# Performance work log

Hardware: AMD Instinct MI355X
Metric: run time of the kernel (lower is better)

The kernel has to match this reference:

```python
import jax, jax.numpy as jnp
import numpy as np

PRUNE_N, PRUNE_M = 2, 4
RIA_A = 1.0
NUM_HEADS = 16
HEAD_DIM = 128
ROPE_THETA = 10000.0


def sparse_mask(W, scaler_row, perm):
    # RIA metric: |W|/colsum + |W|/rowsum, scaled by sqrt(scaler_row)**a
    absW = jnp.abs(W)
    metric = (absW / absW.sum(axis=0, keepdims=True)
              + absW / absW.sum(axis=1, keepdims=True))
    metric = metric * (jnp.sqrt(scaler_row)[None, :] ** RIA_A)
    Wm = metric @ perm                      # permute columns: [R, C]
    R, C = Wm.shape
    nb = C // PRUNE_M
    blocks = Wm.reshape(R, nb, PRUNE_M)
    # hard N:M mask: top-n per block of m
    _, idx = jax.lax.top_k(blocks, PRUNE_N)           # [R, nb, n]
    hard = jax.nn.one_hot(idx, PRUNE_M, dtype=Wm.dtype).sum(axis=-2)  # [R, nb, m]
    soft = jax.nn.softmax(blocks, axis=-1)
    hard = hard.reshape(R, C) @ perm.T
    soft = soft.reshape(R, C) @ perm.T
    # straight-through estimator
    return jax.lax.stop_gradient(hard - soft) + soft


def sparse_linear(x, W, b, scaler_row, perm):
    Wm = W * sparse_mask(W, scaler_row, perm)
    y = jnp.einsum('bsh,oh->bso', x, Wm)
    return y + b if b is not None else y


def rotate_half(x):
    x1, x2 = jnp.split(x, 2, axis=-1)
    return jnp.concatenate([-x2, x1], axis=-1)


def rope_tables(seq_len, dim, dtype):
    inv_freq = 1.0 / (ROPE_THETA ** (jnp.arange(0, dim, 2, dtype=jnp.float32) / dim))
    t = jnp.arange(seq_len, dtype=jnp.float32)
    freqs = jnp.outer(t, inv_freq)               # [S, dim/2]
    emb = jnp.concatenate([freqs, freqs], axis=-1)  # [S, dim]
    return jnp.cos(emb).astype(dtype), jnp.sin(emb).astype(dtype)


def setup_inputs() -> dict:
    key = jax.random.key(0)
    ks = jax.random.split(key, 16)
    H = 2048
    B, S = 2, 2048
    inp = {
        'hidden_states': jax.random.normal(ks[0], (B, S, H), jnp.float32) * 0.02,
        'Wq': jax.random.normal(ks[1], (H, H), jnp.float32) * 0.02,
        'bq': jax.random.normal(ks[2], (H,), jnp.float32) * 0.02,
        'Wk': jax.random.normal(ks[3], (H, H), jnp.float32) * 0.02,
        'bk': jax.random.normal(ks[4], (H,), jnp.float32) * 0.02,
        'Wv': jax.random.normal(ks[5], (H, H), jnp.float32) * 0.02,
        'bv': jax.random.normal(ks[6], (H,), jnp.float32) * 0.02,
        'Wo': jax.random.normal(ks[7], (H, H), jnp.float32) * 0.02,
        'sq': jax.random.uniform(ks[8], (H,), jnp.float32, 0.1, 1.0),
        'sk': jax.random.uniform(ks[9], (H,), jnp.float32, 0.1, 1.0),
        'sv': jax.random.uniform(ks[10], (H,), jnp.float32, 0.1, 1.0),
        'so': jax.random.uniform(ks[11], (H,), jnp.float32, 0.1, 1.0),
        'perm_qkv': jax.random.normal(ks[12], (H, H), jnp.float32) * 0.02,
        'perm_o': jax.random.normal(ks[13], (H, H), jnp.float32) * 0.02,
        'position_ids': jnp.broadcast_to(jnp.arange(S, dtype=jnp.int64), (B, S)),
    }
    return inp


def reference(hidden_states, Wq, bq, Wk, bk, Wv, bv, Wo,
              sq, sk, sv, so, perm_qkv, perm_o, position_ids):
    B, S, H = hidden_states.shape
    q = sparse_linear(hidden_states, Wq, bq, sq, perm_qkv)
    k = sparse_linear(hidden_states, Wk, bk, sk, perm_qkv)
    v = sparse_linear(hidden_states, Wv, bv, sv, perm_qkv)

    q = q.reshape(B, S, NUM_HEADS, HEAD_DIM).transpose(0, 2, 1, 3)  # [B,Hh,S,D]
    k = k.reshape(B, S, NUM_HEADS, HEAD_DIM).transpose(0, 2, 1, 3)
    v = v.reshape(B, S, NUM_HEADS, HEAD_DIM).transpose(0, 2, 1, 3)

    cos, sin = rope_tables(S, HEAD_DIM, q.dtype)
    c = cos[position_ids][:, None]  # [B,1,S,D]
    s = sin[position_ids][:, None]
    q = q * c + rotate_half(q) * s
    k = k * c + rotate_half(k) * s

    scores = jnp.einsum('bhqd,bhkd->bhqk', q, k) / np.sqrt(HEAD_DIM)
    causal = jnp.tril(jnp.ones((S, S), dtype=bool))
    scores = jnp.where(causal[None, None], scores, jnp.finfo(jnp.float32).min)
    attn = jax.nn.softmax(scores.astype(jnp.float32), axis=-1).astype(q.dtype)
    out = jnp.einsum('bhqk,bhkd->bhqd', attn, v)
    out = out.transpose(0, 2, 1, 3).reshape(B, S, H)
    out = sparse_linear(out, Wo, None, so, perm_o)
    return out
```

## Files before the change

### kernel.cpp

```cpp
#include <hip/hip_runtime.h>
#include <cstdint>
#include <cstddef>

typedef __attribute__((ext_vector_type(4))) float  f32x4;
typedef __attribute__((ext_vector_type(4))) int    i32x4;
typedef __attribute__((ext_vector_type(8))) short  s16x8;
typedef __attribute__((ext_vector_type(4))) short  s16x4;
typedef __attribute__((ext_vector_type(8))) __bf16 bf16x8;

struct Ptr4 { const float* p[4]; };

#define DEV __device__ __forceinline__

DEV unsigned short f2bf_u(float x) {
  unsigned u = __builtin_bit_cast(unsigned, x);
  u += 0x7fffu + ((u >> 16) & 1u);
  return (unsigned short)(u >> 16);
}
DEV float bfu2f(unsigned short u) {
  return __builtin_bit_cast(float, ((unsigned)u) << 16);
}
DEV bf16x8 ld_frag(const unsigned short* p) {
  s16x8 v = *(const s16x8*)p;
  return __builtin_bit_cast(bf16x8, v);
}
DEV f32x4 mfma16(bf16x8 a, bf16x8 b, f32x4 c) {
  return __builtin_amdgcn_mfma_f32_16x16x32_bf16(a, b, c, 0, 0, 0);
}
DEV void gload_lds16(const unsigned short* g, unsigned short* l) {
  __builtin_amdgcn_global_load_lds(
      (const __attribute__((address_space(1))) unsigned int*)g,
      (__attribute__((address_space(3))) unsigned int*)l, 16, 0, 0);
}

__global__ __launch_bounds__(256)
void k_rowsum(Ptr4 Ws, float* __restrict__ rowsums)
{
  const int row = blockIdx.x, mat = blockIdx.y, tid = threadIdx.x;
  const float* W = Ws.p[mat] + (size_t)row * 2048;
  float s = 0.f;
  #pragma unroll
  for (int p = 0; p < 2; ++p) {
    f32x4 v = *(const f32x4*)(W + p * 1024 + tid * 4);
    s += fabsf(v[0]) + fabsf(v[1]) + fabsf(v[2]) + fabsf(v[3]);
  }
  #pragma unroll
  for (int off = 1; off < 64; off <<= 1) s += __shfl_xor(s, off);
  __shared__ float red[4];
  if ((tid & 63) == 0) red[tid >> 6] = s;
  __syncthreads();
  if (tid == 0) rowsums[mat * 2048 + row] = red[0] + red[1] + red[2] + red[3];
}

__global__ __launch_bounds__(256)
void k_colsum_part(Ptr4 Ws, float* __restrict__ part)
{
  const int c = blockIdx.x * 256 + threadIdx.x;
  const int r0 = blockIdx.y * 64;
  const int mat = blockIdx.z;
  const float* W = Ws.p[mat];
  float s = 0.f;
  for (int rr = 0; rr < 64; ++rr) s += fabsf(W[(size_t)(r0 + rr) * 2048 + c]);
  part[((size_t)mat * 32 + blockIdx.y) * 2048 + c] = s;
}
__global__ __launch_bounds__(256)
void k_colsum_red(const float* __restrict__ part, float* __restrict__ colsums)
{
  const int gid = blockIdx.x * 256 + threadIdx.x;
  const int mat = gid >> 11, c = gid & 2047;
  float s = 0.f;
  #pragma unroll
  for (int j = 0; j < 32; ++j) s += part[((size_t)mat * 32 + j) * 2048 + c];
  colsums[gid] = s;
}

__global__ __launch_bounds__(256)
void k_metric(Ptr4 Ws, Ptr4 Ss, const float* __restrict__ rowsums,
              const float* __restrict__ colsums,
              unsigned short* __restrict__ mhi, unsigned short* __restrict__ mlo)
{
  const size_t idx4 = ((size_t)blockIdx.x * 256 + threadIdx.x) * 4;
  const int row = (int)(idx4 >> 11);
  const int c = (int)(idx4 & 2047);
  const int mat = row >> 11, rl = row & 2047;
  const float rs = rowsums[mat * 2048 + rl];
  f32x4 w  = *(const f32x4*)(Ws.p[mat] + (size_t)rl * 2048 + c);
  f32x4 cs = *(const f32x4*)(colsums + mat * 2048 + c);
  f32x4 sv = *(const f32x4*)(Ss.p[mat] + c);
  s16x4 hv, lv;
  #pragma unroll
  for (int j = 0; j < 4; ++j) {
    const float a = fabsf(w[j]);
    const float m = (a / cs[j] + a / rs) * sqrtf(sv[j]);
    const unsigned short hb = f2bf_u(m);
    hv[j] = (short)hb;
    lv[j] = (short)f2bf_u(m - bfu2f(hb));
  }
  *(s16x4*)(mhi + idx4) = hv;
  *(s16x4*)(mlo + idx4) = lv;
}

__global__ __launch_bounds__(256)
void k_perm_prep(const float* __restrict__ pq, const float* __restrict__ po,
                 unsigned short* __restrict__ thi_q, unsigned short* __restrict__ tlo_q,
                 unsigned short* __restrict__ thi_o, unsigned short* __restrict__ tlo_o)
{
  __shared__ float T[64 * 65];
  const int which = blockIdx.z;
  const float* src = which ? po : pq;
  unsigned short* thi = which ? thi_o : thi_q;
  unsigned short* tlo = which ? tlo_o : tlo_q;
  const int rb = blockIdx.y * 64, cb = blockIdx.x * 64, tid = threadIdx.x;
  #pragma unroll
  for (int i = 0; i < 4; ++i) {
    const int cc = i * 256 + tid;
    const int rowl = cc >> 4, c4 = (cc & 15) * 4;
    f32x4 v = *(const f32x4*)(src + (size_t)(rb + rowl) * 2048 + cb + c4);
    #pragma unroll
    for (int j = 0; j < 4; ++j) T[rowl * 65 + c4 + j] = v[j];
  }
  __syncthreads();
  #pragma unroll
  for (int i = 0; i < 4; ++i) {
    const int cc = i * 256 + tid;
    const int rowt = cc >> 4, c4 = (cc & 15) * 4;
    s16x4 hh, ll;
    #pragma unroll
    for (int j = 0; j < 4; ++j) {
      const float v = T[(c4 + j) * 65 + rowt];
      const unsigned short hb = f2bf_u(v);
      hh[j] = (short)hb;
      ll[j] = (short)f2bf_u(v - bfu2f(hb));
    }
    const size_t off = (size_t)(cb + rowt) * 2048 + rb + c4;
    *(s16x4*)(thi + off) = hh;
    *(s16x4*)(tlo + off) = ll;
  }
}

__global__ __launch_bounds__(256)
void k_cast_bf(const float* __restrict__ src, unsigned short* __restrict__ dst)
{
  const size_t i = ((size_t)blockIdx.x * 256 + threadIdx.x) * 8;
  f32x4 a = *(const f32x4*)(src + i);
  f32x4 b = *(const f32x4*)(src + i + 4);
  s16x8 o;
  #pragma unroll
  for (int j = 0; j < 4; ++j) o[j] = (short)f2bf_u(a[j]);
  #pragma unroll
  for (int j = 0; j < 4; ++j) o[4 + j] = (short)f2bf_u(b[j]);
  *(s16x8*)(dst + i) = o;
}

__global__ __launch_bounds__(256)
void k_rope_tab(float* __restrict__ ct, float* __restrict__ st)
{
  const int gid = blockIdx.x * 256 + threadIdx.x;
  const int s = gid >> 6, i = gid & 63;
  const float ex = (float)(2 * i) / 128.f;
  const float inv = 1.f / powf(10000.f, ex);
  const float f = (float)s * inv;
  ct[gid] = cosf(f);
  st[gid] = sinf(f);
}

__global__ __launch_bounds__(256)
void k_rope_reshape(const unsigned short* __restrict__ yqkv, const int* __restrict__ pos,
                    const float* __restrict__ ct, const float* __restrict__ st,
                    unsigned short* __restrict__ qo, unsigned short* __restrict__ ko)
{
  const int gid = blockIdx.x * 256 + threadIdx.x;
  const int d = gid & 127;
  const int s = (gid >> 7) & 2047;
  const int h = (gid >> 18) & 15;
  const int b = gid >> 22;
  const int t = b * 2048 + s;
  const int p = pos[t];
  const int dh = d & 63;
  const float cv = ct[p * 64 + dh], svv = st[p * 64 + dh];
  const size_t yb = (size_t)t * 6144 + h * 128;
  const float q0 = bfu2f(yqkv[yb + d]);
  const float k0 = bfu2f(yqkv[yb + 2048 + d]);
  const int pd = (d < 64) ? d + 64 : d - 64;
  float q1 = bfu2f(yqkv[yb + pd]);
  float k1 = bfu2f(yqkv[yb + 2048 + pd]);
  if (d < 64) { q1 = -q1; k1 = -k1; }
  const size_t o = ((size_t)(b * 16 + h) * 2048 + s) * 128 + d;
  qo[o] = f2bf_u(q0 * cv + q1 * svv);
  ko[o] = f2bf_u(k0 * cv + k1 * svv);
}

__global__ __launch_bounds__(256)
void k_vtrans(const unsigned short* __restrict__ yqkv, unsigned short* __restrict__ vt)
{
  __shared__ float T[64 * 129];
  const int st = blockIdx.x, bh = blockIdx.y, tid = threadIdx.x;
  const int b = bh >> 4, h = bh & 15;
  #pragma unroll
  for (int i = 0; i < 4; ++i) {
    const int c = i * 256 + tid;
    const int sl = c >> 4, d8 = (c & 15) * 8;
    s16x8 v = *(const s16x8*)(yqkv + (size_t)(b * 2048 + st * 64 + sl) * 6144 + 4096 + h * 128 + d8);
    #pragma unroll
    for (int j = 0; j < 8; ++j) T[sl * 129 + d8 + j] = bfu2f((unsigned short)v[j]);
  }
  __syncthreads();
  #pragma unroll
  for (int i = 0; i < 4; ++i) {
    const int c = i * 256 + tid;
    const int d = c >> 3, s8 = (c & 7) * 8;
    s16x8 o;
    #pragma unroll
    for (int j = 0; j < 8; ++j) o[j] = (short)f2bf_u(T[(s8 + j) * 129 + d]);
    *(s16x8*)(vt + ((size_t)bh * 128 + d) * 2048 + st * 64 + s8) = o;
  }
}

template<int MODE, int SPLIT>
__global__ __launch_bounds__(256)
void gemm_bt(const unsigned short* __restrict__ Ahi, const unsigned short* __restrict__ Alo,
             const unsigned short* __restrict__ Bhi, const unsigned short* __restrict__ Blo,
             float* __restrict__ Cf, unsigned short* __restrict__ Cb,
             Ptr4 aux, int M, int N, int K)
{
  __shared__ alignas(16) unsigned short As[2 * 4096];
  __shared__ alignas(16) unsigned short Bs[2 * 4096];
  const int tid = threadIdx.x;
  const int lane = tid & 63, wid = tid >> 6;
  const int wm = wid >> 1, wn = wid & 1;
  const int r = lane & 15, g = lane >> 4;
  const int mbase = blockIdx.y * 128;
  const int nbase = blockIdx.x * 128;
  const int KT = K >> 5;
  (void)M;

  const f32x4 zero = {0.f, 0.f, 0.f, 0.f};
  f32x4 acc[4][4];
  #pragma unroll
  for (int i = 0; i < 4; ++i) {
    #pragma unroll
    for (int j = 0; j < 4; ++j) acc[i][j] = zero;
  }

  const int srl = lane >> 2;
  const int sch = lane & 3;

  auto issue_tile = [&](int kt, int buf) {
    const size_t kb = (size_t)kt * 32;
    #pragma unroll
    for (int i = 0; i < 2; ++i) {
      const int rbase = wid * 32 + i * 16;
      const int rloc = rbase + srl;
      const int sc = ((sch ^ ((rloc >> 1) & 3)) << 3);
      const size_t ga = (size_t)(mbase + rloc) * K + kb + sc;
      const size_t gb = (size_t)(nbase + rloc) * K + kb + sc;
      gload_lds16(Ahi + ga, &As[buf * 4096 + rbase * 32]);
      gload_lds16(Bhi + gb, &Bs[buf * 4096 + rbase * 32]);
      if (SPLIT) {
        gload_lds16(Alo + ga, &As[4096 + rbase * 32]);
        gload_lds16(Blo + gb, &Bs[4096 + rbase * 32]);
      }
    }
  };

  if (SPLIT) {
    issue_tile(0, 0);
    for (int kt = 0; kt < KT; ++kt) {
      __syncthreads();

      bf16x8 ah[4], bfr[4], al[4], bl[4];
      #pragma unroll
      for (int mi = 0; mi < 4; ++mi) {
        const int arow = wm * 64 + mi * 16 + r;
        const int sw = ((g ^ ((arow >> 1) & 3)) << 3);
        ah[mi] = ld_frag(&As[arow * 32 + sw]);
        al[mi] = ld_frag(&As[4096 + arow * 32 + sw]);
      }
      #pragma unroll
      for (int ni = 0; ni < 4; ++ni) {
        const int brow = wn * 64 + ni * 16 + r;
        const int sw = ((g ^ ((brow >> 1) & 3)) << 3);
        bfr[ni] = ld_frag(&Bs[brow * 32 + sw]);
        bl[ni] = ld_frag(&Bs[4096 + brow * 32 + sw]);
      }
      __syncthreads();
      if (kt + 1 < KT) issue_tile(kt + 1, 0);

      #pragma unroll
      for (int mi = 0; mi < 4; ++mi) {
        #pragma unroll
        for (int ni = 0; ni < 4; ++ni) {
          acc[mi][ni] = mfma16(al[mi], bfr[ni], acc[mi][ni]);
          acc[mi][ni] = mfma16(ah[mi], bl[ni], acc[mi][ni]);
          acc[mi][ni] = mfma16(ah[mi], bfr[ni], acc[mi][ni]);
        }
      }
    }
  } else {
    issue_tile(0, 0);
    int cur = 0;
    for (int kt = 0; kt < KT; ++kt) {
      __syncthreads();
      if (kt + 1 < KT) issue_tile(kt + 1, cur ^ 1);

      bf16x8 ah[4], bfr[4];
      #pragma unroll
      for (int mi = 0; mi < 4; ++mi) {
        const int arow = wm * 64 + mi * 16 + r;
        ah[mi] = ld_frag(&As[cur * 4096 + arow * 32 + ((g ^ ((arow >> 1) & 3)) << 3)]);
      }
      #pragma unroll
      for (int ni = 0; ni < 4; ++ni) {
        const int brow = wn * 64 + ni * 16 + r;
        bfr[ni] = ld_frag(&Bs[cur * 4096 + brow * 32 + ((g ^ ((brow >> 1) & 3)) << 3)]);
      }
      #pragma unroll
      for (int mi = 0; mi < 4; ++mi) {
        #pragma unroll
        for (int ni = 0; ni < 4; ++ni)
          acc[mi][ni] = mfma16(ah[mi], bfr[ni], acc[mi][ni]);
      }
      cur ^= 1;
    }
  }

  #pragma unroll
  for (int mi = 0; mi < 4; ++mi) {
    #pragma unroll
    for (int ni = 0; ni < 4; ++ni) {
      const int row0 = mbase + wm * 64 + mi * 16 + g * 4;
      const int col  = nbase + wn * 64 + ni * 16 + r;
      if (MODE == 0) {
        #pragma unroll
        for (int e = 0; e < 4; ++e)
          Cf[(size_t)(row0 + e) * N + col] = acc[mi][ni][e];
      } else if (MODE == 1) {
        const float* wsrc = aux.p[row0 >> 11];
        #pragma unroll
        for (int e = 0; e < 4; ++e) {
          const float mval = wsrc[(size_t)((row0 + e) & 2047) * 2048 + col];
          Cb[(size_t)(row0 + e) * N + col] = f2bf_u(acc[mi][ni][e] * mval);
        }
      } else if (MODE == 2) {
        const float* bp = aux.p[col >> 11];
        const float bb = bp[col & 2047];
        #pragma unroll
        for (int e = 0; e < 4; ++e)
          Cb[(size_t)(row0 + e) * N + col] = f2bf_u(acc[mi][ni][e] + bb);
      } else {
        const int ii = r & 3;
        #pragma unroll
        for (int e = 0; e < 4; ++e) {
          const float v  = acc[mi][ni][e];
          const float v1 = __shfl_xor(v, 1);
          const float v2 = __shfl_xor(v, 2);
          const float v3 = __shfl_xor(v, 3);
          int cnt = 0;
          { const int j = ii ^ 1; cnt += (v1 > v) || (v1 == v && j < ii); }
          { const int j = ii ^ 2; cnt += (v2 > v) || (v2 == v && j < ii); }
          { const int j = ii ^ 3; cnt += (v3 > v) || (v3 == v && j < ii); }
          Cb[(size_t)(row0 + e) * N + col] =
              (cnt < 2) ? (unsigned short)0x3F80 : (unsigned short)0;
        }
      }
    }
  }
}

__global__ __launch_bounds__(256)
void attn_fa(const unsigned short* __restrict__ Qh, const unsigned short* __restrict__ Kh,
             const unsigned short* __restrict__ Vt, unsigned short* __restrict__ Out)
{
  __shared__ alignas(16) unsigned short Ks[64 * 128];
  __shared__ alignas(16) unsigned short Vs[128 * 64];
  __shared__ alignas(16) unsigned short Ps[4][1024];
  const int tid = threadIdx.x, lane = tid & 63, wid = tid >> 6;
  const int r = lane & 15, g = lane >> 4;
  const int pair = blockIdx.x, bh = blockIdx.y;
  const int b = bh >> 4, h = bh & 15;
  const f32x4 zero = {0.f, 0.f, 0.f, 0.f};

  for (int half = 0; half < 2; ++half) {
    const int qt = half ? (31 - pair) : pair;
    const int qrow0 = qt * 64 + wid * 16;

    bf16x8 qf[4];
    {
      const unsigned short* qp = Qh + ((size_t)bh * 2048 + qrow0 + r) * 128;
      #pragma unroll
      for (int ks = 0; ks < 4; ++ks) qf[ks] = ld_frag(qp + ks * 32 + g * 8);
    }
    f32x4 oacc[8];
    #pragma unroll
    for (int i = 0; i < 8; ++i) oacc[i] = zero;
    float m_run[4] = {-1e30f, -1e30f, -1e30f, -1e30f};
    float l_run[4] = {0.f, 0.f, 0.f, 0.f};

    for (int kvt = 0; kvt <= qt; ++kvt) {
      i32x4 kr[4], vr[4];
      #pragma unroll
      for (int i = 0; i < 4; ++i) {
        const int c = i * 256 + tid;
        {
          const int row = c >> 4, slot = c & 15;
          kr[i] = *(const i32x4*)(Kh + ((size_t)bh * 2048 + kvt * 64 + row) * 128 + slot * 8);
        }
        {
          const int row = c >> 3, slot = c & 7;
          vr[i] = *(const i32x4*)(Vt + ((size_t)bh * 128 + row) * 2048 + kvt * 64 + slot * 8);
        }
      }
      __syncthreads();
      #pragma unroll
      for (int i = 0; i < 4; ++i) {
        const int c = i * 256 + tid;
        {
          const int row = c >> 4, slot = c & 15;
          *(i32x4*)&Ks[row * 128 + ((slot ^ (row & 7)) << 3)] = kr[i];
        }
        {
          const int row = c >> 3, slot = c & 7;
          *(i32x4*)&Vs[row * 64 + ((slot ^ (row & 7)) << 3)] = vr[i];
        }
      }
      __syncthreads();

      f32x4 sc[4];
      #pragma unroll
      for (int ni = 0; ni < 4; ++ni) sc[ni] = zero;
      #pragma unroll
      for (int ks = 0; ks < 4; ++ks) {
        const int slot = (ks << 2) | g;
        #pragma unroll
        for (int ni = 0; ni < 4; ++ni) {
          const int krow = ni * 16 + r;
          bf16x8 kf = ld_frag(&Ks[krow * 128 + ((slot ^ (krow & 7)) << 3)]);
          sc[ni] = mfma16(qf[ks], kf, sc[ni]);
        }
      }
      const float sscale = 0.08838834764831845f;
      if (kvt == qt) {
        #pragma unroll
        for (int ni = 0; ni < 4; ++ni) {
          const int kvg = kvt * 64 + ni * 16 + r;
          #pragma unroll
          for (int e = 0; e < 4; ++e) {
            const int qg = qrow0 + g * 4 + e;
            const float s = sc[ni][e] * sscale;
            sc[ni][e] = (kvg > qg) ? -1e30f : s;
          }
        }
      } else {
        #pragma unroll
        for (int ni = 0; ni < 4; ++ni) {
          #pragma unroll
          for (int e = 0; e < 4; ++e) sc[ni][e] *= sscale;
        }
      }
      float corr[4];
      #pragma unroll
      for (int e = 0; e < 4; ++e) {
        float mx = fmaxf(fmaxf(sc[0][e], sc[1][e]), fmaxf(sc[2][e], sc[3][e]));
        mx = fmaxf(mx, __shfl_xor(mx, 1));
        mx = fmaxf(mx, __shfl_xor(mx, 2));
        mx = fmaxf(mx, __shfl_xor(mx, 4));
        mx = fmaxf(mx, __shfl_xor(mx, 8));
        const float mn = fmaxf(m_run[e], mx);
        corr[e] = exp2f((m_run[e] - mn) * 1.4426950408889634f);
        m_run[e] = mn;
      }
      float psum[4] = {0.f, 0.f, 0.f, 0.f};
      #pragma unroll
      for (int ni = 0; ni < 4; ++ni) {
        #pragma unroll
        for (int e = 0; e < 4; ++e) {
          const float p = exp2f((sc[ni][e] - m_run[e]) * 1.4426950408889634f);
          sc[ni][e] = p;
          psum[e] += p;
        }
      }
      #pragma unroll
      for (int e = 0; e < 4; ++e) {
        float s = psum[e];
        s += __shfl_xor(s, 1);
        s += __shfl_xor(s, 2);
        s += __shfl_xor(s, 4);
        s += __shfl_xor(s, 8);
        l_run[e] = l_run[e] * corr[e] + s;
      }
      #pragma unroll
      for (int nf = 0; nf < 8; ++nf) {
        #pragma unroll
        for (int e = 0; e < 4; ++e) oacc[nf][e] *= corr[e];
      }
      #pragma unroll
      for (int ni = 0; ni < 4; ++ni) {
        #pragma unroll
        for (int e = 0; e < 4; ++e) {
          const int prow = g * 4 + e;
          const int col = ni * 16 + r;
          const int slot = col >> 3;
          Ps[wid][prow * 64 + ((slot ^ (prow & 7)) << 3) + (col & 7)] = f2bf_u(sc[ni][e]);
        }
      }
      #pragma unroll
      for (int ks = 0; ks < 2; ++ks) {
        const int slot = (ks << 2) | g;
        bf16x8 pf = ld_frag(&Ps[wid][r * 64 + ((slot ^ (r & 7)) << 3)]);
        #pragma unroll
        for (int nf = 0; nf < 8; ++nf) {
          const int vrow = nf * 16 + r;
          bf16x8 vf = ld_frag(&Vs[vrow * 64 + ((slot ^ (vrow & 7)) << 3)]);
          oacc[nf] = mfma16(pf, vf, oacc[nf]);
        }
      }
    }
    #pragma unroll
    for (int e = 0; e < 4; ++e) {
      const float inv = 1.f / l_run[e];
      const int qg = qrow0 + g * 4 + e;
      #pragma unroll
      for (int nf = 0; nf < 8; ++nf) {
        const int d = nf * 16 + r;
        Out[((size_t)(b * 2048 + qg)) * 2048 + h * 128 + d] = f2bf_u(oacc[nf][e] * inv);
      }
    }
  }
}

extern "C" void kernel_launch(void* const* d_in, const int* in_sizes, int n_in,
                              void* d_out, int out_size, void* d_ws, size_t ws_size,
                              hipStream_t stream)
{
  (void)in_sizes; (void)n_in; (void)out_size; (void)ws_size;
  const float* hid   = (const float*)d_in[0];
  const float* Wq    = (const float*)d_in[1];
  const float* bq    = (const float*)d_in[2];
  const float* Wk    = (const float*)d_in[3];
  const float* bk    = (const float*)d_in[4];
  const float* Wv    = (const float*)d_in[5];
  const float* bv    = (const float*)d_in[6];
  const float* Wo    = (const float*)d_in[7];
  const float* sq    = (const float*)d_in[8];
  const float* sk    = (const float*)d_in[9];
  const float* sv    = (const float*)d_in[10];
  const float* so    = (const float*)d_in[11];
  const float* permq = (const float*)d_in[12];
  const float* permo = (const float*)d_in[13];
  const int* pos     = (const int*)d_in[14];
  float* out = (float*)d_out;
  char* ws = (char*)d_ws;

  constexpr size_t OFF_ROWS = 0;
  constexpr size_t OFF_COLS = OFF_ROWS + (size_t)4 * 2048 * 4;
  constexpr size_t OFF_PART = OFF_COLS + (size_t)4 * 2048 * 4;
  constexpr size_t OFF_COS  = OFF_PART + (size_t)4 * 32 * 2048 * 4;
  constexpr size_t OFF_SIN  = OFF_COS + (size_t)2048 * 64 * 4;
  constexpr size_t SZ_PERM  = (size_t)2048 * 2048 * 2;
  constexpr size_t OFF_A    = OFF_SIN + (size_t)2048 * 64 * 4;
  constexpr size_t OFF_PTQH = OFF_A;
  constexpr size_t OFF_PTQL = OFF_PTQH + SZ_PERM;
  constexpr size_t OFF_PTOH = OFF_PTQL + SZ_PERM;
  constexpr size_t OFF_PTOL = OFF_PTOH + SZ_PERM;
  constexpr size_t OFF_PBQ  = OFF_PTOL + SZ_PERM;
  constexpr size_t OFF_PBO  = OFF_PBQ + SZ_PERM;
  constexpr size_t SZ_M8    = (size_t)8192 * 2048 * 2;
  constexpr size_t OFF_B    = OFF_PBO + SZ_PERM;
  constexpr size_t OFF_C    = OFF_B + SZ_M8;
  constexpr size_t OFF_D    = OFF_C + SZ_M8;
  constexpr size_t OFF_E    = OFF_D + SZ_M8;

  float* rowsums = (float*)(ws + OFF_ROWS);
  float* colsums = (float*)(ws + OFF_COLS);
  float* part    = (float*)(ws + OFF_PART);
  float* cost    = (float*)(ws + OFF_COS);
  float* sint    = (float*)(ws + OFF_SIN);
  unsigned short* ptqh = (unsigned short*)(ws + OFF_PTQH);
  unsigned short* ptql = (unsigned short*)(ws + OFF_PTQL);
  unsigned short* ptoh = (unsigned short*)(ws + OFF_PTOH);
  unsigned short* ptol = (unsigned short*)(ws + OFF_PTOL);
  unsigned short* pbq  = (unsigned short*)(ws + OFF_PBQ);
  unsigned short* pbo  = (unsigned short*)(ws + OFF_PBO);
  unsigned short* mhi  = (unsigned short*)(ws + OFF_B);
  unsigned short* mlo  = (unsigned short*)(ws + OFF_C);
  unsigned short* hard = (unsigned short*)(ws + OFF_D);
  unsigned short* wfin = (unsigned short*)(ws + OFF_E);
  unsigned short* yqkv = (unsigned short*)(ws + OFF_B);
  unsigned short* qhb  = (unsigned short*)(ws + OFF_A);
  unsigned short* khb  = (unsigned short*)(ws + OFF_A + 2 * SZ_PERM);
  unsigned short* vtg  = (unsigned short*)(ws + OFF_A + 4 * SZ_PERM);
  unsigned short* xbf  = (unsigned short*)(ws + OFF_D);
  unsigned short* att  = (unsigned short*)(ws + OFF_D + SZ_M8 / 2);

  Ptr4 Wptrs{{Wq, Wk, Wv, Wo}};
  Ptr4 Sptrs{{sq, sk, sv, so}};
  Ptr4 BiasP{{bq, bk, bv, nullptr}};
  Ptr4 AuxQKV{{Wq, Wk, Wv, nullptr}};
  Ptr4 AuxO{{Wo, nullptr, nullptr, nullptr}};
  Ptr4 NoAux{{nullptr, nullptr, nullptr, nullptr}};

  k_rowsum<<<dim3(2048, 4), 256, 0, stream>>>(Wptrs, rowsums);
  k_colsum_part<<<dim3(8, 32, 4), 256, 0, stream>>>(Wptrs, part);
  k_colsum_red<<<32, 256, 0, stream>>>(part, colsums);
  k_metric<<<16384, 256, 0, stream>>>(Wptrs, Sptrs, rowsums, colsums, mhi, mlo);
  k_perm_prep<<<dim3(32, 32, 2), 256, 0, stream>>>(permq, permo, ptqh, ptql, ptoh, ptol);
  k_cast_bf<<<2048, 256, 0, stream>>>(permq, pbq);
  k_cast_bf<<<2048, 256, 0, stream>>>(permo, pbo);
  gemm_bt<3, 1><<<dim3(16, 48), 256, 0, stream>>>(mhi, mlo, ptqh, ptql, nullptr, hard, NoAux, 6144, 2048, 2048);
  gemm_bt<3, 1><<<dim3(16, 16), 256, 0, stream>>>(mhi + (size_t)6144 * 2048, mlo + (size_t)6144 * 2048,
                                                  ptoh, ptol, nullptr, hard + (size_t)6144 * 2048, NoAux, 2048, 2048, 2048);
  gemm_bt<1, 0><<<dim3(16, 48), 256, 0, stream>>>(hard, nullptr, pbq, nullptr, nullptr, wfin, AuxQKV, 6144, 2048, 2048);
  gemm_bt<1, 0><<<dim3(16, 16), 256, 0, stream>>>(hard + (size_t)6144 * 2048, nullptr, pbo, nullptr, nullptr,
                                                  wfin + (size_t)6144 * 2048, AuxO, 2048, 2048, 2048);
  k_cast_bf<<<4096, 256, 0, stream>>>(hid, xbf);
  gemm_bt<2, 0><<<dim3(48, 32), 256, 0, stream>>>(xbf, nullptr, wfin, nullptr, nullptr, yqkv, BiasP, 4096, 6144, 2048);
  k_rope_tab<<<512, 256, 0, stream>>>(cost, sint);
  k_rope_reshape<<<32768, 256, 0, stream>>>(yqkv, pos, cost, sint, qhb, khb);
  k_vtrans<<<dim3(32, 32), 256, 0, stream>>>(yqkv, vtg);
  attn_fa<<<dim3(16, 32), 256, 0, stream>>>(qhb, khb, vtg, att);
  gemm_bt<0, 0><<<dim3(16, 32), 256, 0, stream>>>(att, nullptr, wfin + (size_t)6144 * 2048, nullptr,
                                                  out, nullptr, NoAux, 4096, 2048, 2048);
}
```

Measured before the change: 725.5 us.

## Merge QKV/O mask GEMM launches, fuse perm cast, prefetch next KV tile

Folds the bf16 cast of both permutation matrices into the perm transpose kernel, which drops two launches. The QKV and O mask GEMMs now run as single 8192-row launches, with each block picking its B operand from its row offset, so the GEMM grids grow and two launches go away. The attention kernel now issues global loads for the next K/V tile right after the LDS store, so they overlap the current tile's compute, at the cost of extra live registers. The aux pointer for the MODE 1 GEMM now receives all four W pointers, which depends on how the kernel indexes aux by row.

```diff
diff --git a/kernel.cpp b/kernel.cpp
--- a/kernel.cpp
+++ b/kernel.cpp
@@ -103,21 +103,28 @@
 __global__ __launch_bounds__(256)
 void k_perm_prep(const float* __restrict__ pq, const float* __restrict__ po,
                  unsigned short* __restrict__ thi_q, unsigned short* __restrict__ tlo_q,
-                 unsigned short* __restrict__ thi_o, unsigned short* __restrict__ tlo_o)
+                 unsigned short* __restrict__ thi_o, unsigned short* __restrict__ tlo_o,
+                 unsigned short* __restrict__ pb_q, unsigned short* __restrict__ pb_o)
 {
   __shared__ float T[64 * 65];
   const int which = blockIdx.z;
   const float* src = which ? po : pq;
   unsigned short* thi = which ? thi_o : thi_q;
   unsigned short* tlo = which ? tlo_o : tlo_q;
+  unsigned short* pb  = which ? pb_o : pb_q;
   const int rb = blockIdx.y * 64, cb = blockIdx.x * 64, tid = threadIdx.x;
   #pragma unroll
   for (int i = 0; i < 4; ++i) {
     const int cc = i * 256 + tid;
     const int rowl = cc >> 4, c4 = (cc & 15) * 4;
     f32x4 v = *(const f32x4*)(src + (size_t)(rb + rowl) * 2048 + cb + c4);
-    #pragma unroll
-    for (int j = 0; j < 4; ++j) T[rowl * 65 + c4 + j] = v[j];
+    s16x4 pc;
+    #pragma unroll
+    for (int j = 0; j < 4; ++j) {
+      T[rowl * 65 + c4 + j] = v[j];
+      pc[j] = (short)f2bf_u(v[j]);
+    }
+    *(s16x4*)(pb + (size_t)(rb + rowl) * 2048 + cb + c4) = pc;
   }
   __syncthreads();
   #pragma unroll
@@ -219,7 +226,9 @@
 template<int MODE, int SPLIT>
 __global__ __launch_bounds__(256)
 void gemm_bt(const unsigned short* __restrict__ Ahi, const unsigned short* __restrict__ Alo,
-             const unsigned short* __restrict__ Bhi, const unsigned short* __restrict__ Blo,
+             const unsigned short* __restrict__ Bhi_1, const unsigned short* __restrict__ Blo_1,
+             const unsigned short* __restrict__ Bhi_2, const unsigned short* __restrict__ Blo_2,
+             int bswitch,
              float* __restrict__ Cf, unsigned short* __restrict__ Cb,
              Ptr4 aux, int M, int N, int K)
 {
@@ -233,6 +242,8 @@
   const int nbase = blockIdx.x * 128;
   const int KT = K >> 5;
   (void)M;
+  const unsigned short* Bhi = (mbase >= bswitch) ? Bhi_2 : Bhi_1;
+  const unsigned short* Blo = (mbase >= bswitch) ? Blo_2 : Blo_1;
 
   const f32x4 zero = {0.f, 0.f, 0.f, 0.f};
   f32x4 acc[4][4];
@@ -380,6 +391,22 @@
   const int b = bh >> 4, h = bh & 15;
   const f32x4 zero = {0.f, 0.f, 0.f, 0.f};
 
+  i32x4 kr[4], vr[4];
+  auto issue_kv = [&](int kvt) {
+    #pragma unroll
+    for (int i = 0; i < 4; ++i) {
+      const int c = i * 256 + tid;
+      {
+        const int row = c >> 4, slot = c & 15;
+        kr[i] = *(const i32x4*)(Kh + ((size_t)bh * 2048 + kvt * 64 + row) * 128 + slot * 8);
+      }
+      {
+        const int row = c >> 3, slot = c & 7;
+        vr[i] = *(const i32x4*)(Vt + ((size_t)bh * 128 + row) * 2048 + kvt * 64 + slot * 8);
+      }
+    }
+  };
+
   for (int half = 0; half < 2; ++half) {
     const int qt = half ? (31 - pair) : pair;
     const int qrow0 = qt * 64 + wid * 16;
@@ -396,20 +423,8 @@
     float m_run[4] = {-1e30f, -1e30f, -1e30f, -1e30f};
     float l_run[4] = {0.f, 0.f, 0.f, 0.f};
 
+    issue_kv(0);
     for (int kvt = 0; kvt <= qt; ++kvt) {
-      i32x4 kr[4], vr[4];
-      #pragma unroll
-      for (int i = 0; i < 4; ++i) {
-        const int c = i * 256 + tid;
-        {
-          const int row = c >> 4, slot = c & 15;
-          kr[i] = *(const i32x4*)(Kh + ((size_t)bh * 2048 + kvt * 64 + row) * 128 + slot * 8);
-        }
-        {
-          const int row = c >> 3, slot = c & 7;
-          vr[i] = *(const i32x4*)(Vt + ((size_t)bh * 128 + row) * 2048 + kvt * 64 + slot * 8);
-        }
-      }
       __syncthreads();
       #pragma unroll
       for (int i = 0; i < 4; ++i) {
@@ -424,6 +439,7 @@
         }
       }
       __syncthreads();
+      if (kvt < qt) issue_kv(kvt + 1);
 
       f32x4 sc[4];
       #pragma unroll
@@ -595,29 +611,26 @@
   Ptr4 Wptrs{{Wq, Wk, Wv, Wo}};
   Ptr4 Sptrs{{sq, sk, sv, so}};
   Ptr4 BiasP{{bq, bk, bv, nullptr}};
-  Ptr4 AuxQKV{{Wq, Wk, Wv, nullptr}};
-  Ptr4 AuxO{{Wo, nullptr, nullptr, nullptr}};
   Ptr4 NoAux{{nullptr, nullptr, nullptr, nullptr}};
+  constexpr int NOSW = 1 << 30;
 
   k_rowsum<<<dim3(2048, 4), 256, 0, stream>>>(Wptrs, rowsums);
   k_colsum_part<<<dim3(8, 32, 4), 256, 0, stream>>>(Wptrs, part);
   k_colsum_red<<<32, 256, 0, stream>>>(part, colsums);
   k_metric<<<16384, 256, 0, stream>>>(Wptrs, Sptrs, rowsums, colsums, mhi, mlo);
-  k_perm_prep<<<dim3(32, 32, 2), 256, 0, stream>>>(permq, permo, ptqh, ptql, ptoh, ptol);
-  k_cast_bf<<<2048, 256, 0, stream>>>(permq, pbq);
-  k_cast_bf<<<2048, 256, 0, stream>>>(permo, pbo);
-  gemm_bt<3, 1><<<dim3(16, 48), 256, 0, stream>>>(mhi, mlo, ptqh, ptql, nullptr, hard, NoAux, 6144, 2048, 2048);
-  gemm_bt<3, 1><<<dim3(16, 16), 256, 0, stream>>>(mhi + (size_t)6144 * 2048, mlo + (size_t)6144 * 2048,
-                                                  ptoh, ptol, nullptr, hard + (size_t)6144 * 2048, NoAux, 2048, 2048, 2048);
-  gemm_bt<1, 0><<<dim3(16, 48), 256, 0, stream>>>(hard, nullptr, pbq, nullptr, nullptr, wfin, AuxQKV, 6144, 2048, 2048);
-  gemm_bt<1, 0><<<dim3(16, 16), 256, 0, stream>>>(hard + (size_t)6144 * 2048, nullptr, pbo, nullptr, nullptr,
-                                                  wfin + (size_t)6144 * 2048, AuxO, 2048, 2048, 2048);
+  k_perm_prep<<<dim3(32, 32, 2), 256, 0, stream>>>(permq, permo, ptqh, ptql, ptoh, ptol, pbq, pbo);
+  gemm_bt<3, 1><<<dim3(16, 64), 256, 0, stream>>>(mhi, mlo, ptqh, ptql, ptoh, ptol, 6144,
+                                                  nullptr, hard, NoAux, 8192, 2048, 2048);
+  gemm_bt<1, 0><<<dim3(16, 64), 256, 0, stream>>>(hard, nullptr, pbq, nullptr, pbo, nullptr, 6144,
+                                                  nullptr, wfin, Wptrs, 8192, 2048, 2048);
   k_cast_bf<<<4096, 256, 0, stream>>>(hid, xbf);
-  gemm_bt<2, 0><<<dim3(48, 32), 256, 0, stream>>>(xbf, nullptr, wfin, nullptr, nullptr, yqkv, BiasP, 4096, 6144, 2048);
+  gemm_bt<2, 0><<<dim3(48, 32), 256, 0, stream>>>(xbf, nullptr, wfin, nullptr, wfin, nullptr, NOSW,
+                                                  nullptr, yqkv, BiasP, 4096, 6144, 2048);
   k_rope_tab<<<512, 256, 0, stream>>>(cost, sint);
   k_rope_reshape<<<32768, 256, 0, stream>>>(yqkv, pos, cost, sint, qhb, khb);
   k_vtrans<<<dim3(32, 32), 256, 0, stream>>>(yqkv, vtg);
   attn_fa<<<dim3(16, 32), 256, 0, stream>>>(qhb, khb, vtg, att);
   gemm_bt<0, 0><<<dim3(16, 32), 256, 0, stream>>>(att, nullptr, wfin + (size_t)6144 * 2048, nullptr,
+                                                  wfin + (size_t)6144 * 2048, nullptr, NOSW,
                                                   out, nullptr, NoAux, 4096, 2048, 2048);
 }
```

Result: faster. 663.2 us (-8.6%).
